# Optimization experiments

Hardware: AMD Instinct MI355X
Metric: run time of the kernel (lower is better)

## Reference

```python
import jax, jax.numpy as jnp
import numpy as np

D_MODEL = 4096
D_FF = 16384
TOKENS = 4096
K_SEL = 4096
SCALE = 0.02  # keep activations numerically tame


def setup_inputs() -> dict:
    key = jax.random.key(0)
    ks = jax.random.split(key, 6)
    x = jax.random.normal(ks[0], (TOKENS, D_MODEL), dtype=jnp.float32)
    fc1_w = jax.random.normal(ks[1], (D_FF, D_MODEL), dtype=jnp.float32) * SCALE
    bias1 = jax.random.normal(ks[2], (D_FF,), dtype=jnp.float32) * SCALE
    fc2_w_t = jax.random.normal(ks[3], (D_FF, D_MODEL), dtype=jnp.float32) * SCALE
    bias2 = jax.random.normal(ks[4], (D_MODEL,), dtype=jnp.float32) * SCALE
    index_vec = jnp.sort(jax.random.randint(ks[5], (K_SEL,), 0, D_FF, dtype=jnp.int32))
    return {"x": x, "fc1_w": fc1_w, "bias1": bias1, "fc2_w_t": fc2_w_t,
            "bias2": bias2, "index_vec": index_vec}


def reference(x, fc1_w, bias1, fc2_w_t, bias2, index_vec):
    # gather_matmul_col_h: gather selected neuron rows of fc1, GEMM + bias + relu
    w1 = fc1_w[index_vec]                 # [k, d]
    b1 = bias1[index_vec]                 # [k]
    h = jax.nn.relu(jnp.einsum('td,kd->tk', x, w1) + b1)  # [T, k]
    # gather_matmul_row_h: gather selected rows of fc2^T, GEMM + bias
    w2 = fc2_w_t[index_vec]               # [k, out]
    out = jnp.einsum('tk,ko->to', h, w2) + bias2          # [T, out]
    return out
```

## Files before the change

### kernel.cpp

```cpp
#include <hip/hip_runtime.h>
#include <hip/hip_bf16.h>
#include <stdint.h>

#define TOKENS  4096
#define D_MODEL 4096
#define D_FF    16384
#define K_SEL   4096

typedef __attribute__((ext_vector_type(8))) short short8;
typedef __attribute__((ext_vector_type(4))) float float4v;

typedef const __attribute__((address_space(1))) unsigned int* gptr_t;
typedef __attribute__((address_space(3))) unsigned int* lptr_t;

__device__ inline unsigned short f2bf(float f) {
    union { float f; unsigned int u; } v; v.f = f;
    unsigned int r = v.u + 0x7fffu + ((v.u >> 16) & 1u);
    return (unsigned short)(r >> 16);
}

__global__ void gather_cast_kernel(const float* __restrict__ src,
                                   const int* __restrict__ idx,
                                   unsigned short* __restrict__ dst,
                                   int cols) {
    long e = ((long)blockIdx.x * blockDim.x + threadIdx.x) * 8;
    int row = (int)(e / cols);
    int col = (int)(e - (long)row * cols);
    long srow = idx ? (long)idx[row] : (long)row;
    const float4* s = (const float4*)(src + srow * cols + col);
    float4 a = s[0], b = s[1];
    short8 o;
    o[0] = (short)f2bf(a.x); o[1] = (short)f2bf(a.y);
    o[2] = (short)f2bf(a.z); o[3] = (short)f2bf(a.w);
    o[4] = (short)f2bf(b.x); o[5] = (short)f2bf(b.y);
    o[6] = (short)f2bf(b.z); o[7] = (short)f2bf(b.w);
    *(short8*)(dst + e) = o;
}

__global__ void gather_transpose_cast_kernel(const float* __restrict__ src,
                                             const int* __restrict__ idx,
                                             unsigned short* __restrict__ dst,
                                             int srcCols, int rows) {
    __shared__ float tile[32][33];
    int tx = threadIdx.x;
    int ty = threadIdx.y;
    int k0 = blockIdx.x * 32;
    int n0 = blockIdx.y * 32;
#pragma unroll
    for (int r = 0; r < 4; ++r) {
        int k = k0 + ty + r * 8;
        long sr = idx[k];
        tile[ty + r * 8][tx] = src[sr * srcCols + n0 + tx];
    }
    __syncthreads();
#pragma unroll
    for (int r = 0; r < 4; ++r) {
        int n = n0 + ty + r * 8;
        dst[(long)n * rows + k0 + tx] = f2bf(tile[tx][ty + r * 8]);
    }
}

template <int MODE>
__global__ __launch_bounds__(256)
void gemm_nt(const unsigned short* __restrict__ A,
             const unsigned short* __restrict__ B,
             const float* __restrict__ bias,
             const int* __restrict__ bidx,
             void* __restrict__ Cout,
             int M, int N, int K) {
    __shared__ __align__(16) unsigned short As[8 * 128 * 8];
    __shared__ __align__(16) unsigned short Bs[8 * 128 * 8];

    const int tid  = threadIdx.x;
    const int lane = tid & 63;
    const int wave = tid >> 6;
    const int wm = wave >> 1;
    const int wn = wave & 1;
    const int bm = blockIdx.y * 128;
    const int bn = blockIdx.x * 128;

    const unsigned short* aPtr[4];
    const unsigned short* bPtr[4];
    unsigned short* aLds[4];
    unsigned short* bLds[4];
#pragma unroll
    for (int i = 0; i < 4; ++i) {
        int p = i * 256 + tid;
        int q = p >> 7, m = p & 127;
        aPtr[i] = A + (long)(bm + m) * K + q * 8;
        bPtr[i] = B + (long)(bn + m) * K + q * 8;
        aLds[i] = &As[p * 8];
        bLds[i] = &Bs[p * 8];
    }

    float4v acc[4][4];
#pragma unroll
    for (int i = 0; i < 4; ++i)
#pragma unroll
        for (int j = 0; j < 4; ++j)
            acc[i][j] = (float4v)(0.f);

    const int quad = lane >> 4;
    const int lr   = lane & 15;

    for (int k0 = 0; k0 < K; k0 += 64) {
#pragma unroll
        for (int i = 0; i < 4; ++i)
            __builtin_amdgcn_global_load_lds((gptr_t)(aPtr[i] + k0),
                                             (lptr_t)aLds[i], 16, 0, 0);
#pragma unroll
        for (int i = 0; i < 4; ++i)
            __builtin_amdgcn_global_load_lds((gptr_t)(bPtr[i] + k0),
                                             (lptr_t)bLds[i], 16, 0, 0);
        __syncthreads();

#pragma unroll
        for (int kk = 0; kk < 2; ++kk) {
            short8 af[4], bf[4];
            int q = kk * 4 + quad;
#pragma unroll
            for (int i = 0; i < 4; ++i) {
                int m = wm * 64 + i * 16 + lr;
                af[i] = *(const short8*)&As[(q * 128 + m) * 8];
            }
#pragma unroll
            for (int j = 0; j < 4; ++j) {
                int n = wn * 64 + j * 16 + lr;
                bf[j] = *(const short8*)&Bs[(q * 128 + n) * 8];
            }
#pragma unroll
            for (int i = 0; i < 4; ++i)
#pragma unroll
                for (int j = 0; j < 4; ++j)
                    acc[i][j] = __builtin_amdgcn_mfma_f32_16x16x32_bf16(
                        af[i], bf[j], acc[i][j], 0, 0, 0);
        }
        __syncthreads();
    }

#pragma unroll
    for (int i = 0; i < 4; ++i) {
        int rowBase = bm + wm * 64 + i * 16 + quad * 4;
#pragma unroll
        for (int j = 0; j < 4; ++j) {
            int col = bn + wn * 64 + j * 16 + lr;
            float bv = (MODE == 1) ? bias[bidx[col]] : bias[col];
#pragma unroll
            for (int r = 0; r < 4; ++r) {
                float v = acc[i][j][r] + bv;
                long off = (long)(rowBase + r) * N + col;
                if (MODE == 1) {
                    v = v > 0.f ? v : 0.f;
                    ((unsigned short*)Cout)[off] = f2bf(v);
                } else {
                    ((float*)Cout)[off] = v;
                }
            }
        }
    }
}

extern "C" void kernel_launch(void* const* d_in, const int* in_sizes, int n_in,
                              void* d_out, int out_size, void* d_ws, size_t ws_size,
                              hipStream_t stream) {
    const float* x      = (const float*)d_in[0];
    const float* fc1_w  = (const float*)d_in[1];
    const float* bias1  = (const float*)d_in[2];
    const float* fc2_wt = (const float*)d_in[3];
    const float* bias2  = (const float*)d_in[4];
    const int*   idx    = (const int*)d_in[5];

    char* ws = (char*)d_ws;
    unsigned short* Xb   = (unsigned short*)(ws);
    unsigned short* W1g  = (unsigned short*)(ws + ((size_t)32 << 20));
    unsigned short* W2gT = (unsigned short*)(ws + ((size_t)64 << 20));
    unsigned short* H    = (unsigned short*)(ws + ((size_t)96 << 20));

    gather_cast_kernel<<<(TOKENS * D_MODEL / 8) / 256, 256, 0, stream>>>(
        x, nullptr, Xb, D_MODEL);
    gather_cast_kernel<<<(K_SEL * D_MODEL / 8) / 256, 256, 0, stream>>>(
        fc1_w, idx, W1g, D_MODEL);
    gather_transpose_cast_kernel<<<dim3(K_SEL / 32, D_MODEL / 32), dim3(32, 8), 0, stream>>>(
        fc2_wt, idx, W2gT, D_MODEL, K_SEL);
    gemm_nt<1><<<dim3(K_SEL / 128, TOKENS / 128), 256, 0, stream>>>(
        Xb, W1g, bias1, idx, (void*)H, TOKENS, K_SEL, D_MODEL);
    gemm_nt<0><<<dim3(D_MODEL / 128, TOKENS / 128), 256, 0, stream>>>(
        H, W2gT, bias2, nullptr, d_out, TOKENS, D_MODEL, K_SEL);
}
```

Before: 1.019 ms.

## Rewrite GEMM as 256x256 tile with 4-stage async LDS pipeline

Replaces the 128x128, 256-thread GEMM with a 256x256, 512-thread kernel whose K loop runs over a 4-deep ring of LDS buffers filled by global_load_lds, with vmcnt-based waits so loads for step s+3 overlap MFMA work. It adds a swizzled block mapping to improve L2 reuse and s_setprio around the MFMA bursts. The goal is to hide global load latency and raise arithmetic intensity per tile. In exchange it uses 128KB of dynamic LDS and many accumulator registers, and only 256 workgroups run per GEMM, which can leave the GPU underfilled.

```diff
diff --git a/kernel.cpp b/kernel.cpp
--- a/kernel.cpp
+++ b/kernel.cpp
@@ -1,6 +1,6 @@
 #include <hip/hip_runtime.h>
-#include <hip/hip_bf16.h>
 #include <stdint.h>
+#include <type_traits>
 
 #define TOKENS  4096
 #define D_MODEL 4096
@@ -61,86 +61,126 @@
 }
 
 template <int MODE>
-__global__ __launch_bounds__(256)
-void gemm_nt(const unsigned short* __restrict__ A,
-             const unsigned short* __restrict__ B,
-             const float* __restrict__ bias,
-             const int* __restrict__ bidx,
-             void* __restrict__ Cout,
-             int M, int N, int K) {
-    __shared__ __align__(16) unsigned short As[8 * 128 * 8];
-    __shared__ __align__(16) unsigned short Bs[8 * 128 * 8];
+__global__ __launch_bounds__(512)
+void gemm_nt256(const unsigned short* __restrict__ A,
+                const unsigned short* __restrict__ B,
+                const float* __restrict__ bias,
+                const int* __restrict__ bidx,
+                void* __restrict__ Cout,
+                int M, int N, int K) {
+    extern __shared__ unsigned short lds[];
+    unsigned short* AsB = lds;
+    unsigned short* BsB = lds + 32768;
 
     const int tid  = threadIdx.x;
     const int lane = tid & 63;
     const int wave = tid >> 6;
-    const int wm = wave >> 1;
-    const int wn = wave & 1;
-    const int bm = blockIdx.y * 128;
-    const int bn = blockIdx.x * 128;
-
-    const unsigned short* aPtr[4];
-    const unsigned short* bPtr[4];
-    unsigned short* aLds[4];
-    unsigned short* bLds[4];
-#pragma unroll
-    for (int i = 0; i < 4; ++i) {
-        int p = i * 256 + tid;
-        int q = p >> 7, m = p & 127;
-        aPtr[i] = A + (long)(bm + m) * K + q * 8;
-        bPtr[i] = B + (long)(bn + m) * K + q * 8;
-        aLds[i] = &As[p * 8];
-        bLds[i] = &Bs[p * 8];
-    }
-
-    float4v acc[4][4];
-#pragma unroll
-    for (int i = 0; i < 4; ++i)
+    const int wm   = wave >> 2;
+    const int wn   = wave & 3;
+    const int quad = lane >> 4;
+    const int lr   = lane & 15;
+
+    const int nwg  = (int)(gridDim.x * gridDim.y);
+    const int orig = (int)(blockIdx.y * gridDim.x + blockIdx.x);
+    const int swz  = (orig & 7) * (nwg >> 3) + (orig >> 3);
+    const int bx   = swz % (int)gridDim.x;
+    const int by   = swz / (int)gridDim.x;
+    const int bm   = by * 256;
+    const int bn   = bx * 256;
+
+    const unsigned short* aSrc[2];
+    const unsigned short* bSrc[2];
+    int ldsOff[2];
+#pragma unroll
+    for (int i = 0; i < 2; ++i) {
+        int p = i * 512 + tid;
+        int q = p >> 8, m = p & 255;
+        aSrc[i] = A + (long)(bm + m) * K + q * 8;
+        bSrc[i] = B + (long)(bn + m) * K + q * 8;
+        ldsOff[i] = p * 8;
+    }
+
+    float4v acc[8][4];
+#pragma unroll
+    for (int i = 0; i < 8; ++i)
 #pragma unroll
         for (int j = 0; j < 4; ++j)
             acc[i][j] = (float4v)(0.f);
 
-    const int quad = lane >> 4;
-    const int lr   = lane & 15;
-
-    for (int k0 = 0; k0 < K; k0 += 64) {
+    const int NSUB = K >> 5;
+
+    auto stageA = [&](int s) {
+        unsigned short* dst = AsB + (s & 3) * 8192;
+#pragma unroll
+        for (int i = 0; i < 2; ++i)
+            __builtin_amdgcn_global_load_lds((gptr_t)(aSrc[i] + s * 32),
+                                             (lptr_t)(dst + ldsOff[i]), 16, 0, 0);
+    };
+    auto stageB = [&](int s) {
+        unsigned short* dst = BsB + (s & 3) * 8192;
+#pragma unroll
+        for (int i = 0; i < 2; ++i)
+            __builtin_amdgcn_global_load_lds((gptr_t)(bSrc[i] + s * 32),
+                                             (lptr_t)(dst + ldsOff[i]), 16, 0, 0);
+    };
+
+    stageA(0); stageB(0); stageA(1); stageB(1); stageA(2); stageB(2);
+
+    const int rowA = wm * 128 + lr;
+    const int rowB = wn * 64 + lr;
+
+    auto kiter = [&](int s, auto waitc, auto dostage) {
+        constexpr int  W  = decltype(waitc)::value;
+        constexpr bool DS = decltype(dostage)::value;
+        if constexpr (W == 8)
+            asm volatile("s_waitcnt vmcnt(8)\n\ts_barrier" ::: "memory");
+        else if constexpr (W == 4)
+            asm volatile("s_waitcnt vmcnt(4)\n\ts_barrier" ::: "memory");
+        else
+            asm volatile("s_waitcnt vmcnt(0)\n\ts_barrier" ::: "memory");
+
+        const unsigned short* sA = AsB + (s & 3) * 8192;
+        const unsigned short* sB = BsB + (s & 3) * 8192;
+        const unsigned short* pA = sA + (quad * 256 + rowA) * 8;
+        const unsigned short* pB = sB + (quad * 256 + rowB) * 8;
+
+        short8 af[8], bfr[4];
+#pragma unroll
+        for (int i = 0; i < 4; ++i) af[i] = *(const short8*)(pA + i * 128);
+#pragma unroll
+        for (int j = 0; j < 4; ++j) bfr[j] = *(const short8*)(pB + j * 128);
+        if constexpr (DS) stageA(s + 3);
+        __builtin_amdgcn_s_setprio(1);
 #pragma unroll
         for (int i = 0; i < 4; ++i)
-            __builtin_amdgcn_global_load_lds((gptr_t)(aPtr[i] + k0),
-                                             (lptr_t)aLds[i], 16, 0, 0);
-#pragma unroll
-        for (int i = 0; i < 4; ++i)
-            __builtin_amdgcn_global_load_lds((gptr_t)(bPtr[i] + k0),
-                                             (lptr_t)bLds[i], 16, 0, 0);
-        __syncthreads();
-
-#pragma unroll
-        for (int kk = 0; kk < 2; ++kk) {
-            short8 af[4], bf[4];
-            int q = kk * 4 + quad;
-#pragma unroll
-            for (int i = 0; i < 4; ++i) {
-                int m = wm * 64 + i * 16 + lr;
-                af[i] = *(const short8*)&As[(q * 128 + m) * 8];
-            }
-#pragma unroll
-            for (int j = 0; j < 4; ++j) {
-                int n = wn * 64 + j * 16 + lr;
-                bf[j] = *(const short8*)&Bs[(q * 128 + n) * 8];
-            }
-#pragma unroll
-            for (int i = 0; i < 4; ++i)
-#pragma unroll
-                for (int j = 0; j < 4; ++j)
-                    acc[i][j] = __builtin_amdgcn_mfma_f32_16x16x32_bf16(
-                        af[i], bf[j], acc[i][j], 0, 0, 0);
-        }
-        __syncthreads();
-    }
-
-#pragma unroll
-    for (int i = 0; i < 4; ++i) {
-        int rowBase = bm + wm * 64 + i * 16 + quad * 4;
+#pragma unroll
+            for (int j = 0; j < 4; ++j)
+                acc[i][j] = __builtin_amdgcn_mfma_f32_16x16x32_bf16(
+                    af[i], bfr[j], acc[i][j], 0, 0, 0);
+        __builtin_amdgcn_s_setprio(0);
+
+#pragma unroll
+        for (int i = 0; i < 4; ++i) af[4 + i] = *(const short8*)(pA + 512 + i * 128);
+        if constexpr (DS) stageB(s + 3);
+        __builtin_amdgcn_s_setprio(1);
+#pragma unroll
+        for (int i = 4; i < 8; ++i)
+#pragma unroll
+            for (int j = 0; j < 4; ++j)
+                acc[i][j] = __builtin_amdgcn_mfma_f32_16x16x32_bf16(
+                    af[i], bfr[j], acc[i][j], 0, 0, 0);
+        __builtin_amdgcn_s_setprio(0);
+    };
+
+    for (int s = 0; s < NSUB - 3; ++s)
+        kiter(s, std::integral_constant<int, 8>{}, std::true_type{});
+    kiter(NSUB - 3, std::integral_constant<int, 8>{}, std::false_type{});
+    kiter(NSUB - 2, std::integral_constant<int, 4>{}, std::false_type{});
+    kiter(NSUB - 1, std::integral_constant<int, 0>{}, std::false_type{});
+
+#pragma unroll
+    for (int i = 0; i < 8; ++i) {
+        int rowBase = bm + wm * 128 + i * 16 + quad * 4;
 #pragma unroll
         for (int j = 0; j < 4; ++j) {
             int col = bn + wn * 64 + j * 16 + lr;
@@ -170,6 +210,15 @@
     const float* bias2  = (const float*)d_in[4];
     const int*   idx    = (const int*)d_in[5];
 
+    static bool inited = false;
+    if (!inited) {
+        hipFuncSetAttribute(reinterpret_cast<const void*>(&gemm_nt256<1>),
+                            hipFuncAttributeMaxDynamicSharedMemorySize, 131072);
+        hipFuncSetAttribute(reinterpret_cast<const void*>(&gemm_nt256<0>),
+                            hipFuncAttributeMaxDynamicSharedMemorySize, 131072);
+        inited = true;
+    }
+
     char* ws = (char*)d_ws;
     unsigned short* Xb   = (unsigned short*)(ws);
     unsigned short* W1g  = (unsigned short*)(ws + ((size_t)32 << 20));
@@ -182,8 +231,8 @@
         fc1_w, idx, W1g, D_MODEL);
     gather_transpose_cast_kernel<<<dim3(K_SEL / 32, D_MODEL / 32), dim3(32, 8), 0, stream>>>(
         fc2_wt, idx, W2gT, D_MODEL, K_SEL);
-    gemm_nt<1><<<dim3(K_SEL / 128, TOKENS / 128), 256, 0, stream>>>(
+    gemm_nt256<1><<<dim3(K_SEL / 256, TOKENS / 256), 512, 131072, stream>>>(
         Xb, W1g, bias1, idx, (void*)H, TOKENS, K_SEL, D_MODEL);
-    gemm_nt<0><<<dim3(D_MODEL / 128, TOKENS / 128), 256, 0, stream>>>(
+    gemm_nt256<0><<<dim3(D_MODEL / 256, TOKENS / 256), 512, 131072, stream>>>(
         H, W2gT, bias2, nullptr, d_out, TOKENS, D_MODEL, K_SEL);
 }
```

Result: faster. 851.8 us (-16.4%).
